# Kernel optimization log

Hardware: AMD Instinct MI355X
Metric: run time of the kernel (lower is better)

## Reference

```python
import jax, jax.numpy as jnp
import numpy as np

BS, Z, NOBJ = 16384, 512, 64


def setup_inputs() -> dict:
    key = jax.random.key(0)
    ks = jax.random.split(key, 12)
    din = Z + 4  # z concatenated with bounds (x_size = 0)

    def lin(k, i, o):
        kw, kb = jax.random.split(k)
        w = jax.random.normal(kw, (i, o), jnp.float32) * (1.0 / np.sqrt(i))
        b = jax.random.normal(kb, (o,), jnp.float32) * 0.01
        return w, b

    W1, c1 = lin(ks[0], din, 512)
    W2, c2 = lin(ks[1], 512, 256)
    W3, c3 = lin(ks[2], 256, 128)
    W4, c4 = lin(ks[3], 128, 64)
    W5, c5 = lin(ks[4], 64, NOBJ * 4)
    z = jax.random.normal(ks[5], (BS, Z), jnp.float32)
    # room bounds [x_min, y_min, x_max, y_max]; must allow gaps >= 1
    bounds = jnp.array([0.0, 0.0, 40.0, 40.0], jnp.float32)
    return {"z": z, "bounds": bounds,
            "W1": W1, "c1": c1, "W2": W2, "c2": c2, "W3": W3, "c3": c3,
            "W4": W4, "c4": c4, "W5": W5, "c5": c5}


def _lrelu(v):
    return jnp.where(v > 0, v, 0.2 * v)


def _solve_axis(pp, pg, lo, hi):
    """Exact KKT solution of: min (x-pp)^2 + (g-pg)^2  s.t. x>=lo, g>=1, x+g<=hi.
    Returns (x, w) with w = x + g. Matches the parabolic QP per object/axis."""
    x0 = jnp.maximum(pp, lo)          # box projection (lower bounds only)
    g0 = jnp.maximum(pg, 1.0)
    t = 0.5 * (hi - pp - pg)          # projection of (pp,pg) onto line x+g=hi
    xl = jnp.clip(pp + t, lo, hi - 1.0)
    over = (x0 + g0) > hi             # coupling constraint active?
    x = jnp.where(over, xl, x0)
    g = jnp.where(over, hi - xl, g0)
    return x, x + g


def reference(z, bounds, W1, c1, W2, c2, W3, c3, W4, c4, W5, c5):
    bs = z.shape[0]
    bnd = jnp.broadcast_to(bounds, (bs, 4))
    h = jnp.concatenate([z, bnd], axis=1)          # (bs, z_size+4)
    h = _lrelu(h @ W1 + c1)                        # dropout treated as eval/identity
    h = _lrelu(h @ W2 + c2)
    h = _lrelu(h @ W3 + c3)
    h = _lrelu(h @ W4 + c4)
    p = (h @ W5 + c5).reshape(bs, NOBJ, 4)         # per-object params [px, py, pw, ph]
    px, py, pw, ph = p[..., 0], p[..., 1], p[..., 2], p[..., 3]
    b0, b1, b2, b3 = bounds[0], bounds[1], bounds[2], bounds[3]
    # QP objective: sum (x-px)^2+(y-py)^2+((w-x)-pw)^2+((h-y)-ph)^2
    # s.t. x>=b0, y>=b1, w<=b2, h<=b3, x<=w-1, y<=h-1. Separable per object/axis.
    xs, ws = _solve_axis(px, pw, b0, b2)
    ys, hs = _solve_axis(py, ph, b1, b3)
    return jnp.stack([xs, ys, ws, hs], axis=-1)    # (bs, num_objs, 4)
```

## Files before the change

kernel.cpp:

```cpp
#include <hip/hip_runtime.h>


#define MROWS 16384

typedef __attribute__((ext_vector_type(8))) short bf16x8;
typedef __attribute__((ext_vector_type(4))) float floatx4;

__device__ __forceinline__ unsigned short f2bf(float x) {
    union { float f; unsigned u; } c; c.f = x;
    unsigned r = c.u + 0x7fffu + ((c.u >> 16) & 1u);
    return (unsigned short)(r >> 16);
}
__device__ __forceinline__ float bf2f(unsigned short b) {
    union { unsigned u; float f; } c; c.u = ((unsigned)b) << 16;
    return c.f;
}

__global__ __launch_bounds__(256) void pack_wt(
    const float* __restrict__ W1, unsigned short* __restrict__ T1,
    const float* __restrict__ W2, unsigned short* __restrict__ T2,
    const float* __restrict__ W3, unsigned short* __restrict__ T3,
    const float* __restrict__ W4, unsigned short* __restrict__ T4)
{
    const float* W; unsigned short* T; int Kreal, KS, nshift;
    switch (blockIdx.y) {
        case 0:  W = W1; T = T1; Kreal = 516; KS = 17; nshift = 9; break;
        case 1:  W = W2; T = T2; Kreal = 512; KS = 16; nshift = 8; break;
        case 2:  W = W3; T = T3; Kreal = 256; KS = 8;  nshift = 7; break;
        default: W = W4; T = T4; Kreal = 128; KS = 4;  nshift = 6; break;
    }
    const int N = 1 << nshift;
    const int idx = blockIdx.x * 256 + threadIdx.x;
    if (idx >= N * KS * 32) return;
    const int k = idx >> nshift;
    const int n = idx & (N - 1);
    const unsigned short v = (k < Kreal) ? f2bf(W[idx]) : (unsigned short)0;
    const int ntile = n >> 4, m_l = n & 15;
    const int ks = k >> 5, quad = (k >> 3) & 3, e = k & 7;
    T[(size_t)(((ntile * KS + ks) * 64) + quad * 16 + m_l) * 8 + e] = v;
}

#define OFF_H1   0
#define OFF_MISC 16640
#define OFF_H3   0
#define LDS_TOT  25088
#define LDA1S    72
#define LD_H1    520
#define LD_H2    264
#define LD_H3    136
#define LD_H4    72

template<int NF, int KSTEPS>
__device__ __forceinline__ void layer_gemm(
    unsigned short* lds, int offA, int lda, int offC, int ldc,
    const unsigned short* __restrict__ Wt,
    const float* __restrict__ bias, int wid, int lane)
{
    const int m_l = lane & 15, quad = lane >> 4;
    const unsigned short* __restrict__ Wl =
        Wt + ((size_t)(wid * NF) * KSTEPS * 64 + lane) * 8;
    floatx4 acc[2][NF];
    #pragma unroll
    for (int i = 0; i < 2; ++i)
        #pragma unroll
        for (int j = 0; j < NF; ++j)
            acc[i][j] = (floatx4){0.f, 0.f, 0.f, 0.f};

    #pragma unroll
    for (int ks = 0; ks < KSTEPS; ++ks) {
        const bf16x8 a0 = *(const bf16x8*)&lds[offA + (m_l     ) * lda + ks*32 + quad*8];
        const bf16x8 a1 = *(const bf16x8*)&lds[offA + (m_l + 16) * lda + ks*32 + quad*8];
        #pragma unroll
        for (int j = 0; j < NF; ++j) {
            const bf16x8 b = *(const bf16x8*)(Wl + (size_t)(j * KSTEPS + ks) * 512);
            acc[0][j] = __builtin_amdgcn_mfma_f32_16x16x32_bf16(a0, b, acc[0][j], 0, 0, 0);
            acc[1][j] = __builtin_amdgcn_mfma_f32_16x16x32_bf16(a1, b, acc[1][j], 0, 0, 0);
        }
    }
    #pragma unroll
    for (int j = 0; j < NF; ++j) {
        const int col = wid * (NF * 16) + j * 16 + m_l;
        const float bv = bias[col];
        #pragma unroll
        for (int i = 0; i < 2; ++i)
            #pragma unroll
            for (int r = 0; r < 4; ++r) {
                float v = acc[i][j][r] + bv;
                v = v > 0.f ? v : 0.2f * v;
                lds[offC + (i*16 + quad*4 + r) * ldc + col] = f2bf(v);
            }
    }
}

__global__ __launch_bounds__(256, 3) void fused_mlp_qp(
    const float* __restrict__ z, const float* __restrict__ bounds,
    const unsigned short* __restrict__ Wt1, const float* __restrict__ c1,
    const unsigned short* __restrict__ Wt2, const float* __restrict__ c2,
    const unsigned short* __restrict__ Wt3, const float* __restrict__ c3,
    const unsigned short* __restrict__ Wt4, const float* __restrict__ c4,
    const float* __restrict__ W5, const float* __restrict__ c5,
    float* __restrict__ out)
{
    __shared__ unsigned short lds[LDS_TOT];
    const int tid  = threadIdx.x;
    const int wid  = tid >> 6, lane = tid & 63;
    const int m_l  = lane & 15, quad = lane >> 4;
    const int bm   = blockIdx.x * 32;

    floatx4 acc1[2][8];
    #pragma unroll
    for (int i = 0; i < 2; ++i)
        #pragma unroll
        for (int j = 0; j < 8; ++j)
            acc1[i][j] = (floatx4){0.f, 0.f, 0.f, 0.f};

    const int srow = tid >> 3;
    const int skl  = (tid & 7) * 8;
    const float* __restrict__ zrow = z + (size_t)(bm + srow) * 512 + skl;
    const unsigned short* __restrict__ W1l = Wt1 + ((size_t)(wid * 8) * 17 * 64 + lane) * 8;

    {
        const float4 p0 = *(const float4*)(zrow + 0);
        const float4 p1 = *(const float4*)(zrow + 4);
        unsigned short t[8] = {f2bf(p0.x), f2bf(p0.y), f2bf(p0.z), f2bf(p0.w),
                               f2bf(p1.x), f2bf(p1.y), f2bf(p1.z), f2bf(p1.w)};
        *(uint4*)&lds[OFF_MISC + srow * LDA1S + skl] = *(uint4*)t;
    }

    for (int c = 0; c < 8; ++c) {
        float4 q0 = {0.f,0.f,0.f,0.f}, q1 = {0.f,0.f,0.f,0.f};
        if (c + 1 < 8) {
            q0 = *(const float4*)(zrow + (c + 1) * 64);
            q1 = *(const float4*)(zrow + (c + 1) * 64 + 4);
        }
        __syncthreads();
        const int off = OFF_MISC + (c & 1) * (32 * LDA1S);
        #pragma unroll
        for (int ks = 0; ks < 2; ++ks) {
            const bf16x8 a0 = *(const bf16x8*)&lds[off + (m_l     ) * LDA1S + ks*32 + quad*8];
            const bf16x8 a1 = *(const bf16x8*)&lds[off + (m_l + 16) * LDA1S + ks*32 + quad*8];
            #pragma unroll
            for (int j = 0; j < 8; ++j) {
                const bf16x8 b = *(const bf16x8*)(W1l + (size_t)(j * 17 + c*2 + ks) * 512);
                acc1[0][j] = __builtin_amdgcn_mfma_f32_16x16x32_bf16(a0, b, acc1[0][j], 0, 0, 0);
                acc1[1][j] = __builtin_amdgcn_mfma_f32_16x16x32_bf16(a1, b, acc1[1][j], 0, 0, 0);
            }
        }
        __syncthreads();
        if (c + 1 < 8) {
            unsigned short t[8] = {f2bf(q0.x), f2bf(q0.y), f2bf(q0.z), f2bf(q0.w),
                                   f2bf(q1.x), f2bf(q1.y), f2bf(q1.z), f2bf(q1.w)};
            *(uint4*)&lds[OFF_MISC + ((c + 1) & 1) * (32 * LDA1S) + srow * LDA1S + skl] = *(uint4*)t;
        } else {
            const int frow = tid >> 3;
            const int fkl  = (tid & 7) * 4;
            unsigned short t[4];
            #pragma unroll
            for (int i = 0; i < 4; ++i) {
                const int gk = 512 + fkl + i;
                t[i] = (gk < 516) ? f2bf(bounds[gk - 512]) : (unsigned short)0;
            }
            *(uint2*)&lds[OFF_MISC + frow * LDA1S + fkl] = *(uint2*)t;
        }
    }
    __syncthreads();
    {
        const bf16x8 a0 = *(const bf16x8*)&lds[OFF_MISC + (m_l     ) * LDA1S + quad*8];
        const bf16x8 a1 = *(const bf16x8*)&lds[OFF_MISC + (m_l + 16) * LDA1S + quad*8];
        #pragma unroll
        for (int j = 0; j < 8; ++j) {
            const bf16x8 b = *(const bf16x8*)(W1l + (size_t)(j * 17 + 16) * 512);
            acc1[0][j] = __builtin_amdgcn_mfma_f32_16x16x32_bf16(a0, b, acc1[0][j], 0, 0, 0);
            acc1[1][j] = __builtin_amdgcn_mfma_f32_16x16x32_bf16(a1, b, acc1[1][j], 0, 0, 0);
        }
    }
    #pragma unroll
    for (int j = 0; j < 8; ++j) {
        const int col = wid*128 + j*16 + m_l;
        const float bv = c1[col];
        #pragma unroll
        for (int i = 0; i < 2; ++i)
            #pragma unroll
            for (int r = 0; r < 4; ++r) {
                float v = acc1[i][j][r] + bv;
                v = v > 0.f ? v : 0.2f * v;
                lds[OFF_H1 + (i*16 + quad*4 + r) * LD_H1 + col] = f2bf(v);
            }
    }
    __syncthreads();

    layer_gemm<4,16>(lds, OFF_H1,   LD_H1, OFF_MISC, LD_H2, Wt2, c2, wid, lane);
    __syncthreads();
    layer_gemm<2,8 >(lds, OFF_MISC, LD_H2, OFF_H3,   LD_H3, Wt3, c3, wid, lane);
    __syncthreads();
    layer_gemm<1,4 >(lds, OFF_H3,   LD_H3, OFF_MISC, LD_H4, Wt4, c4, wid, lane);
    __syncthreads();

    const float4 cc = ((const float4*)c5)[lane];
    float ax[8], ay[8], aw[8], ah[8];
    #pragma unroll
    for (int r = 0; r < 8; ++r) { ax[r] = cc.x; ay[r] = cc.y; aw[r] = cc.z; ah[r] = cc.w; }
    const float4* __restrict__ W5v = (const float4*)W5;
    const int rbase = wid * 8;

    #pragma unroll 2
    for (int k4 = 0; k4 < 64; k4 += 4) {
        unsigned short hs[8][4];
        #pragma unroll
        for (int r = 0; r < 8; ++r) {
            const ushort4 t = *(const ushort4*)&lds[OFF_MISC + (rbase + r) * LD_H4 + k4];
            hs[r][0] = t.x; hs[r][1] = t.y; hs[r][2] = t.z; hs[r][3] = t.w;
        }
        #pragma unroll
        for (int kk = 0; kk < 4; ++kk) {
            const float4 w = W5v[(size_t)(k4 + kk) * 64 + lane];
            #pragma unroll
            for (int r = 0; r < 8; ++r) {
                const float h = bf2f(hs[r][kk]);
                ax[r] = fmaf(h, w.x, ax[r]);
                ay[r] = fmaf(h, w.y, ay[r]);
                aw[r] = fmaf(h, w.z, aw[r]);
                ah[r] = fmaf(h, w.w, ah[r]);
            }
        }
    }

    const float b0 = bounds[0], b1 = bounds[1], b2 = bounds[2], b3 = bounds[3];
    #pragma unroll
    for (int r = 0; r < 8; ++r) {
        float xs, wo, ys, ho;
        {
            const float px = ax[r], pw = aw[r];
            const float x0 = fmaxf(px, b0);
            const float g0 = fmaxf(pw, 1.0f);
            const float t  = 0.5f * (b2 - px - pw);
            const float xl = fminf(fmaxf(px + t, b0), b2 - 1.0f);
            const bool over = (x0 + g0) > b2;
            const float x = over ? xl : x0;
            const float g = over ? (b2 - xl) : g0;
            xs = x; wo = x + g;
        }
        {
            const float py = ay[r], ph = ah[r];
            const float x0 = fmaxf(py, b1);
            const float g0 = fmaxf(ph, 1.0f);
            const float t  = 0.5f * (b3 - py - ph);
            const float xl = fminf(fmaxf(py + t, b1), b3 - 1.0f);
            const bool over = (x0 + g0) > b3;
            const float x = over ? xl : x0;
            const float g = over ? (b3 - xl) : g0;
            ys = x; ho = x + g;
        }
        float4 o; o.x = xs; o.y = ys; o.z = wo; o.w = ho;
        ((float4*)out)[(size_t)(bm + rbase + r) * 64 + lane] = o;
    }
}

extern "C" void kernel_launch(void* const* d_in, const int* in_sizes, int n_in,
                              void* d_out, int out_size, void* d_ws, size_t ws_size,
                              hipStream_t stream) {
    const float* z      = (const float*)d_in[0];
    const float* bounds = (const float*)d_in[1];
    const float* W1 = (const float*)d_in[2];
    const float* c1 = (const float*)d_in[3];
    const float* W2 = (const float*)d_in[4];
    const float* c2 = (const float*)d_in[5];
    const float* W3 = (const float*)d_in[6];
    const float* c3 = (const float*)d_in[7];
    const float* W4 = (const float*)d_in[8];
    const float* c4 = (const float*)d_in[9];
    const float* W5 = (const float*)d_in[10];
    const float* c5 = (const float*)d_in[11];
    float* out = (float*)d_out;

    unsigned short* ws  = (unsigned short*)d_ws;
    unsigned short* Wt1 = ws;
    unsigned short* Wt2 = Wt1 + 278528;
    unsigned short* Wt3 = Wt2 + 131072;
    unsigned short* Wt4 = Wt3 + 32768;

    pack_wt<<<dim3(1088, 4), 256, 0, stream>>>(W1, Wt1, W2, Wt2, W3, Wt3, W4, Wt4);
    fused_mlp_qp<<<dim3(MROWS / 32), 256, 0, stream>>>(
        z, bounds, Wt1, c1, Wt2, c2, Wt3, c3, Wt4, c4, W5, c5, out);
}
```

Measured before the change: 137.3 us.

## Stage layer-1 input in two wide halves and software-pipeline weight loads

Layer 1 now stages z in two 256-column halves rather than eight 64-column chunks, which cuts the number of block barriers. B-fragment weight loads across all GEMM layers and the W5 loads in the final layer are register double-buffered (prefetched one step ahead). Bounds are loaded once as a float4. Occupancy hint drops from 3 to 2 blocks per CU to make room for the extra registers, which risks less latency hiding across waves.

```diff
diff --git a/kernel.cpp b/kernel.cpp
--- a/kernel.cpp
+++ b/kernel.cpp
@@ -44,7 +44,7 @@
 #define OFF_MISC 16640
 #define OFF_H3   0
 #define LDS_TOT  25088
-#define LDA1S    72
+#define LD_STG   264
 #define LD_H1    520
 #define LD_H2    264
 #define LD_H3    136
@@ -66,15 +66,44 @@
         for (int j = 0; j < NF; ++j)
             acc[i][j] = (floatx4){0.f, 0.f, 0.f, 0.f};
 
-    #pragma unroll
-    for (int ks = 0; ks < KSTEPS; ++ks) {
-        const bf16x8 a0 = *(const bf16x8*)&lds[offA + (m_l     ) * lda + ks*32 + quad*8];
-        const bf16x8 a1 = *(const bf16x8*)&lds[offA + (m_l + 16) * lda + ks*32 + quad*8];
-        #pragma unroll
-        for (int j = 0; j < NF; ++j) {
-            const bf16x8 b = *(const bf16x8*)(Wl + (size_t)(j * KSTEPS + ks) * 512);
-            acc[0][j] = __builtin_amdgcn_mfma_f32_16x16x32_bf16(a0, b, acc[0][j], 0, 0, 0);
-            acc[1][j] = __builtin_amdgcn_mfma_f32_16x16x32_bf16(a1, b, acc[1][j], 0, 0, 0);
+    if constexpr (NF * KSTEPS <= 16) {
+        bf16x8 b[NF * KSTEPS];
+        #pragma unroll
+        for (int t = 0; t < NF * KSTEPS; ++t)
+            b[t] = *(const bf16x8*)(Wl + (size_t)t * 512);
+        #pragma unroll
+        for (int ks = 0; ks < KSTEPS; ++ks) {
+            const bf16x8 a0 = *(const bf16x8*)&lds[offA + (m_l     ) * lda + ks*32 + quad*8];
+            const bf16x8 a1 = *(const bf16x8*)&lds[offA + (m_l + 16) * lda + ks*32 + quad*8];
+            #pragma unroll
+            for (int j = 0; j < NF; ++j) {
+                acc[0][j] = __builtin_amdgcn_mfma_f32_16x16x32_bf16(a0, b[j*KSTEPS+ks], acc[0][j], 0, 0, 0);
+                acc[1][j] = __builtin_amdgcn_mfma_f32_16x16x32_bf16(a1, b[j*KSTEPS+ks], acc[1][j], 0, 0, 0);
+            }
+        }
+    } else {
+        bf16x8 bc[NF], bn[NF];
+        #pragma unroll
+        for (int j = 0; j < NF; ++j)
+            bc[j] = *(const bf16x8*)(Wl + (size_t)(j * KSTEPS) * 512);
+        #pragma unroll
+        for (int ks = 0; ks < KSTEPS; ++ks) {
+            if (ks + 1 < KSTEPS) {
+                #pragma unroll
+                for (int j = 0; j < NF; ++j)
+                    bn[j] = *(const bf16x8*)(Wl + (size_t)(j * KSTEPS + ks + 1) * 512);
+            }
+            const bf16x8 a0 = *(const bf16x8*)&lds[offA + (m_l     ) * lda + ks*32 + quad*8];
+            const bf16x8 a1 = *(const bf16x8*)&lds[offA + (m_l + 16) * lda + ks*32 + quad*8];
+            #pragma unroll
+            for (int j = 0; j < NF; ++j) {
+                acc[0][j] = __builtin_amdgcn_mfma_f32_16x16x32_bf16(a0, bc[j], acc[0][j], 0, 0, 0);
+                acc[1][j] = __builtin_amdgcn_mfma_f32_16x16x32_bf16(a1, bc[j], acc[1][j], 0, 0, 0);
+            }
+            if (ks + 1 < KSTEPS) {
+                #pragma unroll
+                for (int j = 0; j < NF; ++j) bc[j] = bn[j];
+            }
         }
     }
     #pragma unroll
@@ -92,7 +121,7 @@
     }
 }
 
-__global__ __launch_bounds__(256, 3) void fused_mlp_qp(
+__global__ __launch_bounds__(256, 2) void fused_mlp_qp(
     const float* __restrict__ z, const float* __restrict__ bounds,
     const unsigned short* __restrict__ Wt1, const float* __restrict__ c1,
     const unsigned short* __restrict__ Wt2, const float* __restrict__ c2,
@@ -107,6 +136,8 @@
     const int m_l  = lane & 15, quad = lane >> 4;
     const int bm   = blockIdx.x * 32;
 
+    const float4 bnd = *(const float4*)bounds;
+
     floatx4 acc1[2][8];
     #pragma unroll
     for (int i = 0; i < 2; ++i)
@@ -115,63 +146,81 @@
             acc1[i][j] = (floatx4){0.f, 0.f, 0.f, 0.f};
 
     const int srow = tid >> 3;
-    const int skl  = (tid & 7) * 8;
-    const float* __restrict__ zrow = z + (size_t)(bm + srow) * 512 + skl;
+    const int sc4  = (tid & 7) * 4;
+    const float* __restrict__ zb = z + (size_t)(bm + srow) * 512 + sc4;
     const unsigned short* __restrict__ W1l = Wt1 + ((size_t)(wid * 8) * 17 * 64 + lane) * 8;
 
+    float4 zr[8];
+    #pragma unroll
+    for (int i = 0; i < 8; ++i) zr[i] = *(const float4*)(zb + i * 32);
+    #pragma unroll
+    for (int i = 0; i < 8; ++i) {
+        unsigned short t4[4] = {f2bf(zr[i].x), f2bf(zr[i].y), f2bf(zr[i].z), f2bf(zr[i].w)};
+        *(uint2*)&lds[OFF_MISC + srow * LD_STG + sc4 + i * 32] = *(uint2*)t4;
+    }
+    bf16x8 bc[8], bn[8];
+    #pragma unroll
+    for (int j = 0; j < 8; ++j)
+        bc[j] = *(const bf16x8*)(W1l + (size_t)(j * 17) * 512);
+    #pragma unroll
+    for (int i = 0; i < 8; ++i) zr[i] = *(const float4*)(zb + 256 + i * 32);
+    __syncthreads();
+
+    #pragma unroll
+    for (int ks = 0; ks < 8; ++ks) {
+        #pragma unroll
+        for (int j = 0; j < 8; ++j)
+            bn[j] = *(const bf16x8*)(W1l + (size_t)(j * 17 + ks + 1) * 512);
+        const bf16x8 a0 = *(const bf16x8*)&lds[OFF_MISC + (m_l     ) * LD_STG + ks*32 + quad*8];
+        const bf16x8 a1 = *(const bf16x8*)&lds[OFF_MISC + (m_l + 16) * LD_STG + ks*32 + quad*8];
+        #pragma unroll
+        for (int j = 0; j < 8; ++j) {
+            acc1[0][j] = __builtin_amdgcn_mfma_f32_16x16x32_bf16(a0, bc[j], acc1[0][j], 0, 0, 0);
+            acc1[1][j] = __builtin_amdgcn_mfma_f32_16x16x32_bf16(a1, bc[j], acc1[1][j], 0, 0, 0);
+        }
+        #pragma unroll
+        for (int j = 0; j < 8; ++j) bc[j] = bn[j];
+    }
+    __syncthreads();
+    #pragma unroll
+    for (int i = 0; i < 8; ++i) {
+        unsigned short t4[4] = {f2bf(zr[i].x), f2bf(zr[i].y), f2bf(zr[i].z), f2bf(zr[i].w)};
+        *(uint2*)&lds[OFF_MISC + srow * LD_STG + sc4 + i * 32] = *(uint2*)t4;
+    }
+    __syncthreads();
+
+    #pragma unroll
+    for (int ks = 8; ks < 16; ++ks) {
+        #pragma unroll
+        for (int j = 0; j < 8; ++j)
+            bn[j] = *(const bf16x8*)(W1l + (size_t)(j * 17 + ks + 1) * 512);
+        const bf16x8 a0 = *(const bf16x8*)&lds[OFF_MISC + (m_l     ) * LD_STG + (ks-8)*32 + quad*8];
+        const bf16x8 a1 = *(const bf16x8*)&lds[OFF_MISC + (m_l + 16) * LD_STG + (ks-8)*32 + quad*8];
+        #pragma unroll
+        for (int j = 0; j < 8; ++j) {
+            acc1[0][j] = __builtin_amdgcn_mfma_f32_16x16x32_bf16(a0, bc[j], acc1[0][j], 0, 0, 0);
+            acc1[1][j] = __builtin_amdgcn_mfma_f32_16x16x32_bf16(a1, bc[j], acc1[1][j], 0, 0, 0);
+        }
+        #pragma unroll
+        for (int j = 0; j < 8; ++j) bc[j] = bn[j];
+    }
+    __syncthreads();
     {
-        const float4 p0 = *(const float4*)(zrow + 0);
-        const float4 p1 = *(const float4*)(zrow + 4);
-        unsigned short t[8] = {f2bf(p0.x), f2bf(p0.y), f2bf(p0.z), f2bf(p0.w),
-                               f2bf(p1.x), f2bf(p1.y), f2bf(p1.z), f2bf(p1.w)};
-        *(uint4*)&lds[OFF_MISC + srow * LDA1S + skl] = *(uint4*)t;
-    }
-
-    for (int c = 0; c < 8; ++c) {
-        float4 q0 = {0.f,0.f,0.f,0.f}, q1 = {0.f,0.f,0.f,0.f};
-        if (c + 1 < 8) {
-            q0 = *(const float4*)(zrow + (c + 1) * 64);
-            q1 = *(const float4*)(zrow + (c + 1) * 64 + 4);
-        }
-        __syncthreads();
-        const int off = OFF_MISC + (c & 1) * (32 * LDA1S);
-        #pragma unroll
-        for (int ks = 0; ks < 2; ++ks) {
-            const bf16x8 a0 = *(const bf16x8*)&lds[off + (m_l     ) * LDA1S + ks*32 + quad*8];
-            const bf16x8 a1 = *(const bf16x8*)&lds[off + (m_l + 16) * LDA1S + ks*32 + quad*8];
-            #pragma unroll
-            for (int j = 0; j < 8; ++j) {
-                const bf16x8 b = *(const bf16x8*)(W1l + (size_t)(j * 17 + c*2 + ks) * 512);
-                acc1[0][j] = __builtin_amdgcn_mfma_f32_16x16x32_bf16(a0, b, acc1[0][j], 0, 0, 0);
-                acc1[1][j] = __builtin_amdgcn_mfma_f32_16x16x32_bf16(a1, b, acc1[1][j], 0, 0, 0);
-            }
-        }
-        __syncthreads();
-        if (c + 1 < 8) {
-            unsigned short t[8] = {f2bf(q0.x), f2bf(q0.y), f2bf(q0.z), f2bf(q0.w),
-                                   f2bf(q1.x), f2bf(q1.y), f2bf(q1.z), f2bf(q1.w)};
-            *(uint4*)&lds[OFF_MISC + ((c + 1) & 1) * (32 * LDA1S) + srow * LDA1S + skl] = *(uint4*)t;
-        } else {
-            const int frow = tid >> 3;
-            const int fkl  = (tid & 7) * 4;
-            unsigned short t[4];
-            #pragma unroll
-            for (int i = 0; i < 4; ++i) {
-                const int gk = 512 + fkl + i;
-                t[i] = (gk < 516) ? f2bf(bounds[gk - 512]) : (unsigned short)0;
-            }
-            *(uint2*)&lds[OFF_MISC + frow * LDA1S + fkl] = *(uint2*)t;
-        }
+        const int frow = tid >> 3;
+        const int fkl  = (tid & 7) * 4;
+        unsigned short t4[4] = {0, 0, 0, 0};
+        if (fkl == 0) { t4[0] = f2bf(bnd.x); t4[1] = f2bf(bnd.y);
+                        t4[2] = f2bf(bnd.z); t4[3] = f2bf(bnd.w); }
+        *(uint2*)&lds[OFF_MISC + frow * LD_STG + fkl] = *(uint2*)t4;
     }
     __syncthreads();
     {
-        const bf16x8 a0 = *(const bf16x8*)&lds[OFF_MISC + (m_l     ) * LDA1S + quad*8];
-        const bf16x8 a1 = *(const bf16x8*)&lds[OFF_MISC + (m_l + 16) * LDA1S + quad*8];
+        const bf16x8 a0 = *(const bf16x8*)&lds[OFF_MISC + (m_l     ) * LD_STG + quad*8];
+        const bf16x8 a1 = *(const bf16x8*)&lds[OFF_MISC + (m_l + 16) * LD_STG + quad*8];
         #pragma unroll
         for (int j = 0; j < 8; ++j) {
-            const bf16x8 b = *(const bf16x8*)(W1l + (size_t)(j * 17 + 16) * 512);
-            acc1[0][j] = __builtin_amdgcn_mfma_f32_16x16x32_bf16(a0, b, acc1[0][j], 0, 0, 0);
-            acc1[1][j] = __builtin_amdgcn_mfma_f32_16x16x32_bf16(a1, b, acc1[1][j], 0, 0, 0);
+            acc1[0][j] = __builtin_amdgcn_mfma_f32_16x16x32_bf16(a0, bc[j], acc1[0][j], 0, 0, 0);
+            acc1[1][j] = __builtin_amdgcn_mfma_f32_16x16x32_bf16(a1, bc[j], acc1[1][j], 0, 0, 0);
         }
     }
     #pragma unroll
@@ -203,8 +252,16 @@
     const float4* __restrict__ W5v = (const float4*)W5;
     const int rbase = wid * 8;
 
-    #pragma unroll 2
+    float4 wv[4], wn[4];
+    #pragma unroll
+    for (int kk = 0; kk < 4; ++kk) wv[kk] = W5v[(size_t)kk * 64 + lane];
+
     for (int k4 = 0; k4 < 64; k4 += 4) {
+        if (k4 + 4 < 64) {
+            #pragma unroll
+            for (int kk = 0; kk < 4; ++kk)
+                wn[kk] = W5v[(size_t)(k4 + 4 + kk) * 64 + lane];
+        }
         unsigned short hs[8][4];
         #pragma unroll
         for (int r = 0; r < 8; ++r) {
@@ -213,19 +270,22 @@
         }
         #pragma unroll
         for (int kk = 0; kk < 4; ++kk) {
-            const float4 w = W5v[(size_t)(k4 + kk) * 64 + lane];
             #pragma unroll
             for (int r = 0; r < 8; ++r) {
                 const float h = bf2f(hs[r][kk]);
-                ax[r] = fmaf(h, w.x, ax[r]);
-                ay[r] = fmaf(h, w.y, ay[r]);
-                aw[r] = fmaf(h, w.z, aw[r]);
-                ah[r] = fmaf(h, w.w, ah[r]);
-            }
-        }
-    }
-
-    const float b0 = bounds[0], b1 = bounds[1], b2 = bounds[2], b3 = bounds[3];
+                ax[r] = fmaf(h, wv[kk].x, ax[r]);
+                ay[r] = fmaf(h, wv[kk].y, ay[r]);
+                aw[r] = fmaf(h, wv[kk].z, aw[r]);
+                ah[r] = fmaf(h, wv[kk].w, ah[r]);
+            }
+        }
+        if (k4 + 4 < 64) {
+            #pragma unroll
+            for (int kk = 0; kk < 4; ++kk) wv[kk] = wn[kk];
+        }
+    }
+
+    const float b0 = bnd.x, b1 = bnd.y, b2 = bnd.z, b3 = bnd.w;
     #pragma unroll
     for (int r = 0; r < 8; ++r) {
         float xs, wo, ys, ho;
```

After: 148.4 us. +8.1%, slower.

## Double rows per block with 2x4 wave grid sharing weight tiles

Applied to the files above, without the earlier changes.

Each block now handles 64 rows with 512 threads instead of 32 rows with 256 threads. The 8 waves form a 2x4 grid: two row groups, each paired with four column slices. Waves in the same column slice read the same packed weight fragments, so each weight load from global memory or cache serves twice as many rows. In exchange the shared-memory footprint roughly doubles, the launch drops to 256 larger blocks (about one per CU), and occupancy and latency hiding may change.

```diff
diff --git a/kernel.cpp b/kernel.cpp
--- a/kernel.cpp
+++ b/kernel.cpp
@@ -41,10 +41,11 @@
 }
 
 #define OFF_H1   0
-#define OFF_MISC 16640
+#define OFF_MISC 33280
 #define OFF_H3   0
-#define LDS_TOT  25088
-#define LDA1S    72
+#define LDS_TOT  50176
+#define LD_STG   72
+#define STG_BUF  4608
 #define LD_H1    520
 #define LD_H2    264
 #define LD_H3    136
@@ -54,11 +55,11 @@
 __device__ __forceinline__ void layer_gemm(
     unsigned short* lds, int offA, int lda, int offC, int ldc,
     const unsigned short* __restrict__ Wt,
-    const float* __restrict__ bias, int wid, int lane)
+    const float* __restrict__ bias, int wn, int mrow, int lane)
 {
     const int m_l = lane & 15, quad = lane >> 4;
     const unsigned short* __restrict__ Wl =
-        Wt + ((size_t)(wid * NF) * KSTEPS * 64 + lane) * 8;
+        Wt + ((size_t)(wn * NF) * KSTEPS * 64 + lane) * 8;
     floatx4 acc[2][NF];
     #pragma unroll
     for (int i = 0; i < 2; ++i)
@@ -68,8 +69,8 @@
 
     #pragma unroll
     for (int ks = 0; ks < KSTEPS; ++ks) {
-        const bf16x8 a0 = *(const bf16x8*)&lds[offA + (m_l     ) * lda + ks*32 + quad*8];
-        const bf16x8 a1 = *(const bf16x8*)&lds[offA + (m_l + 16) * lda + ks*32 + quad*8];
+        const bf16x8 a0 = *(const bf16x8*)&lds[offA + (mrow + m_l     ) * lda + ks*32 + quad*8];
+        const bf16x8 a1 = *(const bf16x8*)&lds[offA + (mrow + m_l + 16) * lda + ks*32 + quad*8];
         #pragma unroll
         for (int j = 0; j < NF; ++j) {
             const bf16x8 b = *(const bf16x8*)(Wl + (size_t)(j * KSTEPS + ks) * 512);
@@ -79,7 +80,7 @@
     }
     #pragma unroll
     for (int j = 0; j < NF; ++j) {
-        const int col = wid * (NF * 16) + j * 16 + m_l;
+        const int col = wn * (NF * 16) + j * 16 + m_l;
         const float bv = bias[col];
         #pragma unroll
         for (int i = 0; i < 2; ++i)
@@ -87,12 +88,12 @@
             for (int r = 0; r < 4; ++r) {
                 float v = acc[i][j][r] + bv;
                 v = v > 0.f ? v : 0.2f * v;
-                lds[offC + (i*16 + quad*4 + r) * ldc + col] = f2bf(v);
-            }
-    }
-}
-
-__global__ __launch_bounds__(256, 3) void fused_mlp_qp(
+                lds[offC + (mrow + i*16 + quad*4 + r) * ldc + col] = f2bf(v);
+            }
+    }
+}
+
+__global__ __launch_bounds__(512, 2) void fused_mlp_qp(
     const float* __restrict__ z, const float* __restrict__ bounds,
     const unsigned short* __restrict__ Wt1, const float* __restrict__ c1,
     const unsigned short* __restrict__ Wt2, const float* __restrict__ c2,
@@ -104,8 +105,10 @@
     __shared__ unsigned short lds[LDS_TOT];
     const int tid  = threadIdx.x;
     const int wid  = tid >> 6, lane = tid & 63;
+    const int wm   = wid >> 2, wn = wid & 3;
+    const int mrow = wm * 32;
     const int m_l  = lane & 15, quad = lane >> 4;
-    const int bm   = blockIdx.x * 32;
+    const int bm   = blockIdx.x * 64;
 
     floatx4 acc1[2][8];
     #pragma unroll
@@ -117,14 +120,14 @@
     const int srow = tid >> 3;
     const int skl  = (tid & 7) * 8;
     const float* __restrict__ zrow = z + (size_t)(bm + srow) * 512 + skl;
-    const unsigned short* __restrict__ W1l = Wt1 + ((size_t)(wid * 8) * 17 * 64 + lane) * 8;
+    const unsigned short* __restrict__ W1l = Wt1 + ((size_t)(wn * 8) * 17 * 64 + lane) * 8;
 
     {
         const float4 p0 = *(const float4*)(zrow + 0);
         const float4 p1 = *(const float4*)(zrow + 4);
         unsigned short t[8] = {f2bf(p0.x), f2bf(p0.y), f2bf(p0.z), f2bf(p0.w),
                                f2bf(p1.x), f2bf(p1.y), f2bf(p1.z), f2bf(p1.w)};
-        *(uint4*)&lds[OFF_MISC + srow * LDA1S + skl] = *(uint4*)t;
+        *(uint4*)&lds[OFF_MISC + srow * LD_STG + skl] = *(uint4*)t;
     }
 
     for (int c = 0; c < 8; ++c) {
@@ -134,11 +137,11 @@
             q1 = *(const float4*)(zrow + (c + 1) * 64 + 4);
         }
         __syncthreads();
-        const int off = OFF_MISC + (c & 1) * (32 * LDA1S);
+        const int off = OFF_MISC + (c & 1) * STG_BUF;
         #pragma unroll
         for (int ks = 0; ks < 2; ++ks) {
-            const bf16x8 a0 = *(const bf16x8*)&lds[off + (m_l     ) * LDA1S + ks*32 + quad*8];
-            const bf16x8 a1 = *(const bf16x8*)&lds[off + (m_l + 16) * LDA1S + ks*32 + quad*8];
+            const bf16x8 a0 = *(const bf16x8*)&lds[off + (mrow + m_l     ) * LD_STG + ks*32 + quad*8];
+            const bf16x8 a1 = *(const bf16x8*)&lds[off + (mrow + m_l + 16) * LD_STG + ks*32 + quad*8];
             #pragma unroll
             for (int j = 0; j < 8; ++j) {
                 const bf16x8 b = *(const bf16x8*)(W1l + (size_t)(j * 17 + c*2 + ks) * 512);
@@ -150,7 +153,7 @@
         if (c + 1 < 8) {
             unsigned short t[8] = {f2bf(q0.x), f2bf(q0.y), f2bf(q0.z), f2bf(q0.w),
                                    f2bf(q1.x), f2bf(q1.y), f2bf(q1.z), f2bf(q1.w)};
-            *(uint4*)&lds[OFF_MISC + ((c + 1) & 1) * (32 * LDA1S) + srow * LDA1S + skl] = *(uint4*)t;
+            *(uint4*)&lds[OFF_MISC + ((c + 1) & 1) * STG_BUF + srow * LD_STG + skl] = *(uint4*)t;
         } else {
             const int frow = tid >> 3;
             const int fkl  = (tid & 7) * 4;
@@ -160,13 +163,13 @@
                 const int gk = 512 + fkl + i;
                 t[i] = (gk < 516) ? f2bf(bounds[gk - 512]) : (unsigned short)0;
             }
-            *(uint2*)&lds[OFF_MISC + frow * LDA1S + fkl] = *(uint2*)t;
+            *(uint2*)&lds[OFF_MISC + frow * LD_STG + fkl] = *(uint2*)t;
         }
     }
     __syncthreads();
     {
-        const bf16x8 a0 = *(const bf16x8*)&lds[OFF_MISC + (m_l     ) * LDA1S + quad*8];
-        const bf16x8 a1 = *(const bf16x8*)&lds[OFF_MISC + (m_l + 16) * LDA1S + quad*8];
+        const bf16x8 a0 = *(const bf16x8*)&lds[OFF_MISC + (mrow + m_l     ) * LD_STG + quad*8];
+        const bf16x8 a1 = *(const bf16x8*)&lds[OFF_MISC + (mrow + m_l + 16) * LD_STG + quad*8];
         #pragma unroll
         for (int j = 0; j < 8; ++j) {
             const bf16x8 b = *(const bf16x8*)(W1l + (size_t)(j * 17 + 16) * 512);
@@ -176,7 +179,7 @@
     }
     #pragma unroll
     for (int j = 0; j < 8; ++j) {
-        const int col = wid*128 + j*16 + m_l;
+        const int col = wn*128 + j*16 + m_l;
         const float bv = c1[col];
         #pragma unroll
         for (int i = 0; i < 2; ++i)
@@ -184,19 +187,20 @@
             for (int r = 0; r < 4; ++r) {
                 float v = acc1[i][j][r] + bv;
                 v = v > 0.f ? v : 0.2f * v;
-                lds[OFF_H1 + (i*16 + quad*4 + r) * LD_H1 + col] = f2bf(v);
-            }
-    }
-    __syncthreads();
-
-    layer_gemm<4,16>(lds, OFF_H1,   LD_H1, OFF_MISC, LD_H2, Wt2, c2, wid, lane);
-    __syncthreads();
-    layer_gemm<2,8 >(lds, OFF_MISC, LD_H2, OFF_H3,   LD_H3, Wt3, c3, wid, lane);
-    __syncthreads();
-    layer_gemm<1,4 >(lds, OFF_H3,   LD_H3, OFF_MISC, LD_H4, Wt4, c4, wid, lane);
-    __syncthreads();
-
-    const float4 cc = ((const float4*)c5)[lane];
+                lds[OFF_H1 + (mrow + i*16 + quad*4 + r) * LD_H1 + col] = f2bf(v);
+            }
+    }
+    __syncthreads();
+
+    layer_gemm<4,16>(lds, OFF_H1,   LD_H1, OFF_MISC, LD_H2, Wt2, c2, wn, mrow, lane);
+    __syncthreads();
+    layer_gemm<2,8 >(lds, OFF_MISC, LD_H2, OFF_H3,   LD_H3, Wt3, c3, wn, mrow, lane);
+    __syncthreads();
+    layer_gemm<1,4 >(lds, OFF_H3,   LD_H3, OFF_MISC, LD_H4, Wt4, c4, wn, mrow, lane);
+    __syncthreads();
+
+    const float4 bnd = *(const float4*)bounds;
+    const float4 cc  = ((const float4*)c5)[lane];
     float ax[8], ay[8], aw[8], ah[8];
     #pragma unroll
     for (int r = 0; r < 8; ++r) { ax[r] = cc.x; ay[r] = cc.y; aw[r] = cc.z; ah[r] = cc.w; }
@@ -225,7 +229,7 @@
         }
     }
 
-    const float b0 = bounds[0], b1 = bounds[1], b2 = bounds[2], b3 = bounds[3];
+    const float b0 = bnd.x, b1 = bnd.y, b2 = bnd.z, b3 = bnd.w;
     #pragma unroll
     for (int r = 0; r < 8; ++r) {
         float xs, wo, ys, ho;
@@ -280,6 +284,6 @@
     unsigned short* Wt4 = Wt3 + 32768;
 
     pack_wt<<<dim3(1088, 4), 256, 0, stream>>>(W1, Wt1, W2, Wt2, W3, Wt3, W4, Wt4);
-    fused_mlp_qp<<<dim3(MROWS / 32), 256, 0, stream>>>(
+    fused_mlp_qp<<<dim3(MROWS / 64), 512, 0, stream>>>(
         z, bounds, Wt1, c1, Wt2, c2, Wt3, c3, Wt4, c4, W5, c5, out);
 }
```

Result: slower. 140.3 us (+2.2%).

## Stage full z tile in LDS and reuse generic layer GEMM for layer 1

Applied to the files above, without the earlier changes.

Layer 1 previously streamed z through a double-buffered 64-column LDS chunk with two barriers per chunk. Now the whole 32x516 bf16 input tile is loaded into LDS up front, and layer 1 goes through the same layer_gemm template as the other layers. This removes the per-chunk barriers and the chunk loop, but drops the overlap of global z loads with MFMA work. It also grows LDS from about 50 KB to about 69 KB per block and lowers the occupancy hint from 3 to 2 blocks per CU.

```diff
diff --git a/kernel.cpp b/kernel.cpp
--- a/kernel.cpp
+++ b/kernel.cpp
@@ -40,15 +40,17 @@
     T[(size_t)(((ntile * KS + ks) * 64) + quad * 16 + m_l) * 8 + e] = v;
 }
 
-#define OFF_H1   0
-#define OFF_MISC 16640
-#define OFF_H3   0
-#define LDS_TOT  25088
-#define LDA1S    72
+#define OFF_ZS   0
+#define LD_ZS    552
+#define OFF_H1   17664
 #define LD_H1    520
+#define OFF_H2   0
 #define LD_H2    264
+#define OFF_H3   17664
 #define LD_H3    136
+#define OFF_H4   8448
 #define LD_H4    72
+#define LDS_TOT  34304
 
 template<int NF, int KSTEPS>
 __device__ __forceinline__ void layer_gemm(
@@ -92,7 +94,7 @@
     }
 }
 
-__global__ __launch_bounds__(256, 3) void fused_mlp_qp(
+__global__ __launch_bounds__(256, 2) void fused_mlp_qp(
     const float* __restrict__ z, const float* __restrict__ bounds,
     const unsigned short* __restrict__ Wt1, const float* __restrict__ c1,
     const unsigned short* __restrict__ Wt2, const float* __restrict__ c2,
@@ -104,96 +106,37 @@
     __shared__ unsigned short lds[LDS_TOT];
     const int tid  = threadIdx.x;
     const int wid  = tid >> 6, lane = tid & 63;
-    const int m_l  = lane & 15, quad = lane >> 4;
     const int bm   = blockIdx.x * 32;
 
-    floatx4 acc1[2][8];
-    #pragma unroll
-    for (int i = 0; i < 2; ++i)
-        #pragma unroll
-        for (int j = 0; j < 8; ++j)
-            acc1[i][j] = (floatx4){0.f, 0.f, 0.f, 0.f};
-
-    const int srow = tid >> 3;
-    const int skl  = (tid & 7) * 8;
-    const float* __restrict__ zrow = z + (size_t)(bm + srow) * 512 + skl;
-    const unsigned short* __restrict__ W1l = Wt1 + ((size_t)(wid * 8) * 17 * 64 + lane) * 8;
+    const float4 bnd = *(const float4*)bounds;
 
     {
-        const float4 p0 = *(const float4*)(zrow + 0);
-        const float4 p1 = *(const float4*)(zrow + 4);
-        unsigned short t[8] = {f2bf(p0.x), f2bf(p0.y), f2bf(p0.z), f2bf(p0.w),
-                               f2bf(p1.x), f2bf(p1.y), f2bf(p1.z), f2bf(p1.w)};
-        *(uint4*)&lds[OFF_MISC + srow * LDA1S + skl] = *(uint4*)t;
-    }
-
-    for (int c = 0; c < 8; ++c) {
-        float4 q0 = {0.f,0.f,0.f,0.f}, q1 = {0.f,0.f,0.f,0.f};
-        if (c + 1 < 8) {
-            q0 = *(const float4*)(zrow + (c + 1) * 64);
-            q1 = *(const float4*)(zrow + (c + 1) * 64 + 4);
-        }
-        __syncthreads();
-        const int off = OFF_MISC + (c & 1) * (32 * LDA1S);
-        #pragma unroll
-        for (int ks = 0; ks < 2; ++ks) {
-            const bf16x8 a0 = *(const bf16x8*)&lds[off + (m_l     ) * LDA1S + ks*32 + quad*8];
-            const bf16x8 a1 = *(const bf16x8*)&lds[off + (m_l + 16) * LDA1S + ks*32 + quad*8];
-            #pragma unroll
-            for (int j = 0; j < 8; ++j) {
-                const bf16x8 b = *(const bf16x8*)(W1l + (size_t)(j * 17 + c*2 + ks) * 512);
-                acc1[0][j] = __builtin_amdgcn_mfma_f32_16x16x32_bf16(a0, b, acc1[0][j], 0, 0, 0);
-                acc1[1][j] = __builtin_amdgcn_mfma_f32_16x16x32_bf16(a1, b, acc1[1][j], 0, 0, 0);
-            }
-        }
-        __syncthreads();
-        if (c + 1 < 8) {
-            unsigned short t[8] = {f2bf(q0.x), f2bf(q0.y), f2bf(q0.z), f2bf(q0.w),
-                                   f2bf(q1.x), f2bf(q1.y), f2bf(q1.z), f2bf(q1.w)};
-            *(uint4*)&lds[OFF_MISC + ((c + 1) & 1) * (32 * LDA1S) + srow * LDA1S + skl] = *(uint4*)t;
-        } else {
-            const int frow = tid >> 3;
-            const int fkl  = (tid & 7) * 4;
-            unsigned short t[4];
-            #pragma unroll
-            for (int i = 0; i < 4; ++i) {
-                const int gk = 512 + fkl + i;
-                t[i] = (gk < 516) ? f2bf(bounds[gk - 512]) : (unsigned short)0;
-            }
-            *(uint2*)&lds[OFF_MISC + frow * LDA1S + fkl] = *(uint2*)t;
-        }
-    }
-    __syncthreads();
-    {
-        const bf16x8 a0 = *(const bf16x8*)&lds[OFF_MISC + (m_l     ) * LDA1S + quad*8];
-        const bf16x8 a1 = *(const bf16x8*)&lds[OFF_MISC + (m_l + 16) * LDA1S + quad*8];
-        #pragma unroll
-        for (int j = 0; j < 8; ++j) {
-            const bf16x8 b = *(const bf16x8*)(W1l + (size_t)(j * 17 + 16) * 512);
-            acc1[0][j] = __builtin_amdgcn_mfma_f32_16x16x32_bf16(a0, b, acc1[0][j], 0, 0, 0);
-            acc1[1][j] = __builtin_amdgcn_mfma_f32_16x16x32_bf16(a1, b, acc1[1][j], 0, 0, 0);
-        }
-    }
-    #pragma unroll
-    for (int j = 0; j < 8; ++j) {
-        const int col = wid*128 + j*16 + m_l;
-        const float bv = c1[col];
-        #pragma unroll
-        for (int i = 0; i < 2; ++i)
-            #pragma unroll
-            for (int r = 0; r < 4; ++r) {
-                float v = acc1[i][j][r] + bv;
-                v = v > 0.f ? v : 0.2f * v;
-                lds[OFF_H1 + (i*16 + quad*4 + r) * LD_H1 + col] = f2bf(v);
-            }
-    }
-    __syncthreads();
-
-    layer_gemm<4,16>(lds, OFF_H1,   LD_H1, OFF_MISC, LD_H2, Wt2, c2, wid, lane);
-    __syncthreads();
-    layer_gemm<2,8 >(lds, OFF_MISC, LD_H2, OFF_H3,   LD_H3, Wt3, c3, wid, lane);
-    __syncthreads();
-    layer_gemm<1,4 >(lds, OFF_H3,   LD_H3, OFF_MISC, LD_H4, Wt4, c4, wid, lane);
+        const float4* __restrict__ zf = (const float4*)(z + (size_t)bm * 512);
+        #pragma unroll
+        for (int i = 0; i < 16; ++i) {
+            const int f   = i * 256 + tid;
+            const int row = f >> 7, c4 = f & 127;
+            const float4 v = zf[f];
+            unsigned short t4[4] = {f2bf(v.x), f2bf(v.y), f2bf(v.z), f2bf(v.w)};
+            *(uint2*)&lds[OFF_ZS + row * LD_ZS + c4 * 4] = *(uint2*)t4;
+        }
+        if (tid < 160) {
+            const int row = tid / 5, j = tid % 5;
+            unsigned short t8[8] = {0,0,0,0,0,0,0,0};
+            if (j == 0) { t8[0] = f2bf(bnd.x); t8[1] = f2bf(bnd.y);
+                          t8[2] = f2bf(bnd.z); t8[3] = f2bf(bnd.w); }
+            *(uint4*)&lds[OFF_ZS + row * LD_ZS + 512 + j * 8] = *(uint4*)t8;
+        }
+    }
+    __syncthreads();
+
+    layer_gemm<8,17>(lds, OFF_ZS, LD_ZS, OFF_H1, LD_H1, Wt1, c1, wid, lane);
+    __syncthreads();
+    layer_gemm<4,16>(lds, OFF_H1, LD_H1, OFF_H2, LD_H2, Wt2, c2, wid, lane);
+    __syncthreads();
+    layer_gemm<2,8 >(lds, OFF_H2, LD_H2, OFF_H3, LD_H3, Wt3, c3, wid, lane);
+    __syncthreads();
+    layer_gemm<1,4 >(lds, OFF_H3, LD_H3, OFF_H4, LD_H4, Wt4, c4, wid, lane);
     __syncthreads();
 
     const float4 cc = ((const float4*)c5)[lane];
@@ -208,7 +151,7 @@
         unsigned short hs[8][4];
         #pragma unroll
         for (int r = 0; r < 8; ++r) {
-            const ushort4 t = *(const ushort4*)&lds[OFF_MISC + (rbase + r) * LD_H4 + k4];
+            const ushort4 t = *(const ushort4*)&lds[OFF_H4 + (rbase + r) * LD_H4 + k4];
             hs[r][0] = t.x; hs[r][1] = t.y; hs[r][2] = t.z; hs[r][3] = t.w;
         }
         #pragma unroll
@@ -225,7 +168,7 @@
         }
     }
 
-    const float b0 = bounds[0], b1 = bounds[1], b2 = bounds[2], b3 = bounds[3];
+    const float b0 = bnd.x, b1 = bnd.y, b2 = bnd.z, b3 = bnd.w;
     #pragma unroll
     for (int r = 0; r < 8; ++r) {
         float xs, wo, ys, ho;
```

Result: faster. 133.5 us (-2.8%).
